# Optimization experiments

Measured on AMD Instinct MI355X. Metric: run time of the kernel, lower is better.

## Reference

```python
import jax, jax.numpy as jnp
import numpy as np

BETA = 1e10  # hard softmax temperature from the original module


def setup_inputs() -> dict:
    key = jax.random.key(0)
    ks = jax.random.split(key, 7)
    bs, nc, units, feat = 128, 1024, 512, 512
    return {
        "x": jax.random.normal(ks[0], (bs, feat), jnp.float32),
        "class_logits": jax.random.normal(ks[1], (bs, nc), jnp.float32),
        "h_states": jax.random.normal(ks[2], (nc, units), jnp.float32) * 0.1,
        "c_states": jax.random.normal(ks[3], (nc, units), jnp.float32) * 0.1,
        "kernel": jax.random.normal(ks[4], (feat, 4 * units), jnp.float32) * 0.05,
        "rec_kernel": jax.random.normal(ks[5], (units, 4 * units), jnp.float32) * 0.05,
        "bias": jnp.zeros((4 * units,), jnp.float32),
    }


def _diff_scatter(A, B, w):
    # A: (nc, u) old class states, B: (bs, u) new states, w: (bs, nc) hard softmax.
    # Faithful to tf version: broadcast to (nc, bs, u), blend, then reduce_max over bs.
    m = w.T[:, :, None]                       # (nc, bs, 1)
    blended = A[:, None, :] * (1.0 - m) + B[None, :, :] * m  # (nc, bs, u)
    return jnp.max(blended, axis=1)           # (nc, u)


def reference(x, class_logits, h_states, c_states, kernel, rec_kernel, bias):
    # diff_gather: softmax-weighted sum over classes == weights @ params
    w = jax.nn.softmax(class_logits * BETA, axis=-1)  # (bs, nc), ~one-hot
    h0 = w @ h_states                                  # (bs, u)
    c0 = w @ c_states                                  # (bs, u)

    # single-step Keras LSTM (seq_len == 1): gate order i, f, c, o
    z = x @ kernel + h0 @ rec_kernel + bias            # (bs, 4u)
    i, f, g, o = jnp.split(z, 4, axis=-1)
    i = jax.nn.sigmoid(i)
    f = jax.nn.sigmoid(f)
    g = jnp.tanh(g)
    o = jax.nn.sigmoid(o)
    c = f * c0 + i * g
    h = o * jnp.tanh(c)                                # LSTM output == h

    new_h = _diff_scatter(h_states, h, w)
    new_c = _diff_scatter(c_states, c, w)
    return h, new_h, new_c
```

## Files before the change

kernel.cpp:

```cpp
#include <hip/hip_runtime.h>
#include <hip/hip_bf16.h>
#include <math.h>

#define BS    128
#define NC    1024
#define UNITS 512
#define FEAT  512
#define FOURU 2048
#define KG    4
#define NT    16

typedef short bf16x8 __attribute__((ext_vector_type(8)));
typedef float f32x4  __attribute__((ext_vector_type(4)));

__device__ __forceinline__ unsigned short bf_rhu(float f) {
    union { float f; unsigned u; } v; v.f = f;
    return (unsigned short)((v.u + 0x8000u) >> 16);
}
__device__ __forceinline__ unsigned pack2(float a, float b) {
    return (unsigned)bf_rhu(a) | ((unsigned)bf_rhu(b) << 16);
}

__global__ __launch_bounds__(256) void argmax_prep_kernel(
    const float* __restrict__ logits, const float* __restrict__ x,
    const float* __restrict__ h_states,
    int* __restrict__ sidx, unsigned* __restrict__ Abf )
{
    int b = blockIdx.x;
    int t = threadIdx.x;
    float best = -INFINITY; int bi = 0;
    for (int i = t; i < NC; i += 256) {
        float v = logits[b * NC + i];
        if (v > best) { best = v; bi = i; }
    }
    for (int off = 32; off > 0; off >>= 1) {
        float ov = __shfl_down(best, off);
        int   oi = __shfl_down(bi, off);
        if (ov > best || (ov == best && oi < bi)) { best = ov; bi = oi; }
    }
    __shared__ float sv[4]; __shared__ int si[4]; __shared__ int sbi;
    int wid = t >> 6;
    if ((t & 63) == 0) { sv[wid] = best; si[wid] = bi; }
    __syncthreads();
    if (t == 0) {
        for (int w = 1; w < 4; ++w)
            if (sv[w] > best || (sv[w] == best && si[w] < bi)) { best = sv[w]; bi = si[w]; }
        sidx[b] = bi;
        sbi = bi;
    }
    __syncthreads();
    int st = t & 127;
    const float* srcrow = (t < 128) ? (x + (long)b * FEAT)
                                    : (h_states + (long)sbi * UNITS);
    float4 v = *(const float4*)(srcrow + st * 4);
    unsigned lo = pack2(v.x, v.y), hi = pack2(v.z, v.w);
    unsigned du = (unsigned)b * 512u + (t < 128 ? 0u : 256u) + (unsigned)st * 2u;
    *(uint2*)(Abf + du) = make_uint2(lo, hi);
}

__global__ __launch_bounds__(256) void gemm_kernel(
    const unsigned short* __restrict__ Abf,
    const float* __restrict__ kern, const float* __restrict__ reck,
    float* __restrict__ z_part)
{
    const int t = threadIdx.x;
    const int wid = t >> 6, lane = t & 63, l15 = lane & 15, quad = lane >> 4;
    const int nt = blockIdx.x, kg = blockIdx.y;
    const int n  = nt * NT + l15;
    const int k0base = kg * 256;
    const float* W  = (kg < 2) ? kern : reck;
    const int wkbase = (kg & 1) * 256;

    f32x4 zero = {0.f, 0.f, 0.f, 0.f};
    f32x4 acc[2] = {zero, zero};

    #pragma unroll
    for (int kstep = 0; kstep < 8; ++kstep) {
        int k0  = k0base + kstep * 32 + quad * 8;
        int wk0 = wkbase + kstep * 32 + quad * 8;

        bf16x8 af[2], wf;
        #pragma unroll
        for (int ms = 0; ms < 2; ++ms) {
            int m = wid * 32 + ms * 16 + l15;
            af[ms] = *(const bf16x8*)(Abf + (long)m * 1024 + k0);
        }
        const float* Wp = W + (long)wk0 * FOURU + n;
        #pragma unroll
        for (int j = 0; j < 8; ++j)
            wf[j] = (short)bf_rhu(Wp[(long)j * FOURU]);

        #pragma unroll
        for (int ms = 0; ms < 2; ++ms)
            acc[ms] = __builtin_amdgcn_mfma_f32_16x16x32_bf16(af[ms], wf, acc[ms], 0, 0, 0);
    }

    float* zp = z_part + (long)kg * BS * FOURU;
    #pragma unroll
    for (int ms = 0; ms < 2; ++ms)
        #pragma unroll
        for (int r = 0; r < 4; ++r) {
            int m = wid * 32 + ms * 16 + quad * 4 + r;
            zp[(long)m * FOURU + n] = acc[ms][r];
        }
}

__global__ __launch_bounds__(256) void scatter_lstm_kernel(
    const float* __restrict__ z_part, const float* __restrict__ bias,
    const float* __restrict__ h_states, const float* __restrict__ c_states,
    const int* __restrict__ sidx,
    float* __restrict__ h_out, float* __restrict__ out_h, float* __restrict__ out_c)
{
    __shared__ int s[BS];
    int t = threadIdx.x;
    if (t < BS) s[t] = sidx[t];
    __syncthreads();
    int j = blockIdx.x >> 1;
    int u = (blockIdx.x & 1) * 256 + t;

    float ah = h_states[(long)j * UNITS + u];
    float ac = c_states[(long)j * UNITS + u];

    float mh = -INFINITY, mc = -INFINITY;
    int count = 0;
    float bi_ = bias[u], bf_ = bias[512 + u], bg_ = bias[1024 + u], bo_ = bias[1536 + u];

    for (int b = 0; b < BS; ++b) {
        if (s[b] == j) {
            ++count;
            float zi = bi_, zf = bf_, zg = bg_, zo = bo_;
            #pragma unroll
            for (int kg = 0; kg < KG; ++kg) {
                const float* zp = z_part + (long)kg * BS * FOURU + (long)b * FOURU;
                zi += zp[u];
                zf += zp[512 + u];
                zg += zp[1024 + u];
                zo += zp[1536 + u];
            }
            float ig = 1.f / (1.f + expf(-zi));
            float fg = 1.f / (1.f + expf(-zf));
            float gg = tanhf(zg);
            float og = 1.f / (1.f + expf(-zo));
            float c  = fg * ac + ig * gg;
            float h  = og * tanhf(c);
            h_out[(long)b * UNITS + u] = h;
            mh = fmaxf(mh, h);
            mc = fmaxf(mc, c);
        }
    }
    out_h[(long)j * UNITS + u] = (count == BS) ? mh : fmaxf(ah, mh);
    out_c[(long)j * UNITS + u] = (count == BS) ? mc : fmaxf(ac, mc);
}

extern "C" void kernel_launch(void* const* d_in, const int* in_sizes, int n_in,
                              void* d_out, int out_size, void* d_ws, size_t ws_size,
                              hipStream_t stream)
{
    (void)in_sizes; (void)n_in; (void)out_size; (void)ws_size;
    const float* x      = (const float*)d_in[0];
    const float* logits = (const float*)d_in[1];
    const float* h_st   = (const float*)d_in[2];
    const float* c_st   = (const float*)d_in[3];
    const float* kern   = (const float*)d_in[4];
    const float* reck   = (const float*)d_in[5];
    const float* bias   = (const float*)d_in[6];

    float* out        = (float*)d_out;
    float* out_h_step = out;
    float* out_newh   = out + BS * UNITS;
    float* out_newc   = out + BS * UNITS + NC * UNITS;

    char*           ws     = (char*)d_ws;
    int*            sidx   = (int*)ws;
    unsigned*       Abf    = (unsigned*)(ws + 4096);
    float*          z_part = (float*)(ws + (1u << 20));

    argmax_prep_kernel<<<BS, 256, 0, stream>>>(logits, x, h_st, sidx, Abf);
    gemm_kernel<<<dim3(128, KG), 256, 0, stream>>>(
        (const unsigned short*)Abf, kern, reck, z_part);
    scatter_lstm_kernel<<<NC * UNITS / 256, 256, 0, stream>>>(
        z_part, bias, h_st, c_st, sidx, out_h_step, out_newh, out_newc);
}
```

Measured before the change: 103.3 us.

## Fuse argmax and bf16 conversion into GEMM, dropping the prep kernel

Removes the separate argmax/prep kernel. GEMM blocks handling the recurrent half now compute each row's argmax from the logits themselves and gather h_states rows directly. A operands are read in fp32 and converted to bf16 on the fly instead of through a staged bf16 buffer. This saves a kernel launch and the intermediate write/read, at the cost of redundant argmax scans in every h-side block and a longer serial pre-GEMM phase.

```diff
diff --git a/kernel.cpp b/kernel.cpp
--- a/kernel.cpp
+++ b/kernel.cpp
@@ -17,75 +17,65 @@
     union { float f; unsigned u; } v; v.f = f;
     return (unsigned short)((v.u + 0x8000u) >> 16);
 }
-__device__ __forceinline__ unsigned pack2(float a, float b) {
-    return (unsigned)bf_rhu(a) | ((unsigned)bf_rhu(b) << 16);
-}
 
-__global__ __launch_bounds__(256) void argmax_prep_kernel(
+__global__ __launch_bounds__(256) void gemm_fused_kernel(
     const float* __restrict__ logits, const float* __restrict__ x,
-    const float* __restrict__ h_states,
-    int* __restrict__ sidx, unsigned* __restrict__ Abf )
-{
-    int b = blockIdx.x;
-    int t = threadIdx.x;
-    float best = -INFINITY; int bi = 0;
-    for (int i = t; i < NC; i += 256) {
-        float v = logits[b * NC + i];
-        if (v > best) { best = v; bi = i; }
-    }
-    for (int off = 32; off > 0; off >>= 1) {
-        float ov = __shfl_down(best, off);
-        int   oi = __shfl_down(bi, off);
-        if (ov > best || (ov == best && oi < bi)) { best = ov; bi = oi; }
-    }
-    __shared__ float sv[4]; __shared__ int si[4]; __shared__ int sbi;
-    int wid = t >> 6;
-    if ((t & 63) == 0) { sv[wid] = best; si[wid] = bi; }
-    __syncthreads();
-    if (t == 0) {
-        for (int w = 1; w < 4; ++w)
-            if (sv[w] > best || (sv[w] == best && si[w] < bi)) { best = sv[w]; bi = si[w]; }
-        sidx[b] = bi;
-        sbi = bi;
-    }
-    __syncthreads();
-    int st = t & 127;
-    const float* srcrow = (t < 128) ? (x + (long)b * FEAT)
-                                    : (h_states + (long)sbi * UNITS);
-    float4 v = *(const float4*)(srcrow + st * 4);
-    unsigned lo = pack2(v.x, v.y), hi = pack2(v.z, v.w);
-    unsigned du = (unsigned)b * 512u + (t < 128 ? 0u : 256u) + (unsigned)st * 2u;
-    *(uint2*)(Abf + du) = make_uint2(lo, hi);
-}
-
-__global__ __launch_bounds__(256) void gemm_kernel(
-    const unsigned short* __restrict__ Abf,
+    const float* __restrict__ h_st,
     const float* __restrict__ kern, const float* __restrict__ reck,
-    float* __restrict__ z_part)
+    int* __restrict__ sidx, float* __restrict__ z_part)
 {
     const int t = threadIdx.x;
     const int wid = t >> 6, lane = t & 63, l15 = lane & 15, quad = lane >> 4;
     const int nt = blockIdx.x, kg = blockIdx.y;
     const int n  = nt * NT + l15;
-    const int k0base = kg * 256;
-    const float* W  = (kg < 2) ? kern : reck;
+    const bool isH = (kg >= 2);
+    const float* W  = isH ? reck : kern;
     const int wkbase = (kg & 1) * 256;
+    const int akbase = isH ? (kg - 2) * 256 : kg * 256;
+
+    int ridx[2] = {0, 0};
+    if (isH) {
+        int r    = wid * 32 + (lane >> 1);
+        int half = lane & 1;
+        const float* lp = logits + (long)r * NC + half * 512;
+        float best = -INFINITY; int bi = 0;
+        #pragma unroll 4
+        for (int i = 0; i < 128; ++i) {
+            float4 v = *(const float4*)(lp + i * 4);
+            if (v.x > best) { best = v.x; bi = i * 4 + 0; }
+            if (v.y > best) { best = v.y; bi = i * 4 + 1; }
+            if (v.z > best) { best = v.z; bi = i * 4 + 2; }
+            if (v.w > best) { best = v.w; bi = i * 4 + 3; }
+        }
+        bi += half * 512;
+        float ov = __shfl_xor(best, 1);
+        int   oi = __shfl_xor(bi, 1);
+        if (ov > best || (ov == best && oi < bi)) { best = ov; bi = oi; }
+        if (nt == 0 && kg == 2 && half == 0) sidx[r] = bi;
+        ridx[0] = __shfl(bi, 2 * l15);
+        ridx[1] = __shfl(bi, 2 * (16 + l15));
+    }
 
     f32x4 zero = {0.f, 0.f, 0.f, 0.f};
     f32x4 acc[2] = {zero, zero};
 
     #pragma unroll
     for (int kstep = 0; kstep < 8; ++kstep) {
-        int k0  = k0base + kstep * 32 + quad * 8;
-        int wk0 = wkbase + kstep * 32 + quad * 8;
-
+        int koff = kstep * 32 + quad * 8;
         bf16x8 af[2], wf;
         #pragma unroll
         for (int ms = 0; ms < 2; ++ms) {
-            int m = wid * 32 + ms * 16 + l15;
-            af[ms] = *(const bf16x8*)(Abf + (long)m * 1024 + k0);
+            const float* ap = isH
+                ? (h_st + (long)ridx[ms] * UNITS + akbase + koff)
+                : (x    + (long)(wid * 32 + ms * 16 + l15) * FEAT + akbase + koff);
+            float4 a0 = *(const float4*)ap;
+            float4 a1 = *(const float4*)(ap + 4);
+            af[ms][0] = (short)bf_rhu(a0.x); af[ms][1] = (short)bf_rhu(a0.y);
+            af[ms][2] = (short)bf_rhu(a0.z); af[ms][3] = (short)bf_rhu(a0.w);
+            af[ms][4] = (short)bf_rhu(a1.x); af[ms][5] = (short)bf_rhu(a1.y);
+            af[ms][6] = (short)bf_rhu(a1.z); af[ms][7] = (short)bf_rhu(a1.w);
         }
-        const float* Wp = W + (long)wk0 * FOURU + n;
+        const float* Wp = W + (long)(wkbase + koff) * FOURU + n;
         #pragma unroll
         for (int j = 0; j < 8; ++j)
             wf[j] = (short)bf_rhu(Wp[(long)j * FOURU]);
@@ -170,14 +160,12 @@
     float* out_newh   = out + BS * UNITS;
     float* out_newc   = out + BS * UNITS + NC * UNITS;
 
-    char*           ws     = (char*)d_ws;
-    int*            sidx   = (int*)ws;
-    unsigned*       Abf    = (unsigned*)(ws + 4096);
-    float*          z_part = (float*)(ws + (1u << 20));
+    char*     ws     = (char*)d_ws;
+    int*      sidx   = (int*)ws;
+    float*    z_part = (float*)(ws + (1u << 20));
 
-    argmax_prep_kernel<<<BS, 256, 0, stream>>>(logits, x, h_st, sidx, Abf);
-    gemm_kernel<<<dim3(128, KG), 256, 0, stream>>>(
-        (const unsigned short*)Abf, kern, reck, z_part);
+    gemm_fused_kernel<<<dim3(128, KG), 256, 0, stream>>>(
+        logits, x, h_st, kern, reck, sidx, z_part);
     scatter_lstm_kernel<<<NC * UNITS / 256, 256, 0, stream>>>(
         z_part, bias, h_st, c_st, sidx, out_h_step, out_newh, out_newc);
 }
```

Result: slower. 119.1 us (+15.3%).
